# Optimization experiments

Measured on AMD Instinct MI355X. Metric: run time of the kernel, lower is better.

The kernel has to match this reference:

```python
import jax, jax.numpy as jnp
import numpy as np

B, N, D = 16, 8192, 768
H = int(D * 4.0)  # mlp hidden
EPS = 1e-6
D_SQRT = D ** (-0.5)


def setup_inputs() -> dict:
    key = jax.random.key(0)
    ks = jax.random.split(key, 6)
    x = jax.random.normal(ks[0], (B, N, D), dtype=jnp.float32)
    # learnable query, trunc-normal std = D**-0.5 (plain normal is fine for a reference)
    query = jax.random.normal(ks[1], (D,), dtype=jnp.float32) * D_SQRT
    ln_gamma = jnp.ones((D,), dtype=jnp.float32)
    ln_beta = jnp.zeros((D,), dtype=jnp.float32)
    w1 = jax.random.normal(ks[2], (D, H), dtype=jnp.float32) * (D ** -0.5)
    b1 = jnp.zeros((H,), dtype=jnp.float32)
    w2 = jax.random.normal(ks[3], (H, D), dtype=jnp.float32) * (H ** -0.5)
    b2 = jnp.zeros((D,), dtype=jnp.float32)
    return {"x": x, "query": query, "ln_gamma": ln_gamma, "ln_beta": ln_beta,
            "w1": w1, "b1": b1, "w2": w2, "b2": b2}


def _layernorm(x, gamma, beta):
    mu = jnp.mean(x, axis=-1, keepdims=True)
    var = jnp.mean(jnp.square(x - mu), axis=-1, keepdims=True)
    return (x - mu) * jax.lax.rsqrt(var + EPS) * gamma + beta


def reference(x, query, ln_gamma, ln_beta, w1, b1, w2, b2):
    # single-query cross attention: attn [B, N]
    attn = jnp.einsum('d,bnd->bn', query, x)
    attn_sm = jax.nn.softmax(attn * D_SQRT, axis=-1)
    pooled = jnp.einsum('bn,bnd->bd', attn_sm, x)  # [B, D]
    h = _layernorm(pooled, ln_gamma, ln_beta)
    h = jax.nn.gelu(h @ w1 + b1, approximate=False) @ w2 + b2
    out = pooled + h
    return out, attn
```

## Files before the change

### kernel.cpp

```cpp
#include <hip/hip_runtime.h>
#include <hip/hip_bf16.h>
#include <math.h>

#define BB 16
#define NN 8192
#define DD 768
#define HH 3072
#define EPSV 1e-6f
#define DSQRT 0.03608439182435161f

#define CHUNKS 64
#define ROWS_PER_BLOCK (NN / CHUNKS)
#define NWAVES 4
#define ROWS_PER_WAVE (ROWS_PER_BLOCK / NWAVES)
#define PSTRIDE 772
#define QQ 4

#define KS1 16
#define KL1 (DD / KS1)
#define KS2 48
#define KL2 (HH / KS2)

__global__ __launch_bounds__(256) void attn_pool_k(
    const float* __restrict__ x, const float* __restrict__ query,
    float* __restrict__ attn_out, float* __restrict__ partials)
{
    const int b     = blockIdx.y;
    const int chunk = blockIdx.x;
    const int tid   = threadIdx.x;
    const int wave  = tid >> 6;
    const int lane  = tid & 63;

    const float4* q4 = (const float4*)query;
    const float4 q0 = q4[lane];
    const float4 q1 = q4[lane + 64];
    const float4 q2 = q4[lane + 128];

    float4 p0 = make_float4(0.f, 0.f, 0.f, 0.f);
    float4 p1 = make_float4(0.f, 0.f, 0.f, 0.f);
    float4 p2 = make_float4(0.f, 0.f, 0.f, 0.f);
    float esum = 0.f;

    const int n0 = chunk * ROWS_PER_BLOCK + wave * ROWS_PER_WAVE;
    const float4* xb = (const float4*)(x + (size_t)b * NN * DD);

    #pragma unroll 2
    for (int r = 0; r < ROWS_PER_WAVE; ++r) {
        const int n = n0 + r;
        const float4* xr = xb + (size_t)n * (DD / 4);
        const float4 v0 = xr[lane];
        const float4 v1 = xr[lane + 64];
        const float4 v2 = xr[lane + 128];

        float s = v0.x * q0.x + v0.y * q0.y + v0.z * q0.z + v0.w * q0.w;
        s += v1.x * q1.x + v1.y * q1.y + v1.z * q1.z + v1.w * q1.w;
        s += v2.x * q2.x + v2.y * q2.y + v2.z * q2.z + v2.w * q2.w;
        #pragma unroll
        for (int off = 32; off > 0; off >>= 1) s += __shfl_xor(s, off);

        if (lane == 0) attn_out[(size_t)b * NN + n] = s;

        const float e = expf(s * DSQRT);
        esum += e;
        p0.x += e * v0.x; p0.y += e * v0.y; p0.z += e * v0.z; p0.w += e * v0.w;
        p1.x += e * v1.x; p1.y += e * v1.y; p1.z += e * v1.z; p1.w += e * v1.w;
        p2.x += e * v2.x; p2.y += e * v2.y; p2.z += e * v2.z; p2.w += e * v2.w;
    }

    __shared__ float lds[NWAVES][PSTRIDE];
    float* my = lds[wave];
    *(float4*)&my[lane * 4]       = p0;
    *(float4*)&my[256 + lane * 4] = p1;
    *(float4*)&my[512 + lane * 4] = p2;
    if (lane == 0) my[768] = esum;
    __syncthreads();

    float* outp = partials + (size_t)(b * CHUNKS + chunk) * PSTRIDE;
    #pragma unroll
    for (int k = 0; k < 3; ++k) {
        const int idx = tid + k * 256;
        outp[idx] = lds[0][idx] + lds[1][idx] + lds[2][idx] + lds[3][idx];
    }
    if (tid == 0) outp[768] = lds[0][768] + lds[1][768] + lds[2][768] + lds[3][768];
}

__global__ __launch_bounds__(256) void qreduce_k(
    const float* __restrict__ partials, float* __restrict__ qsum,
    float* __restrict__ qden)
{
    const int slice = blockIdx.x % 3;
    const int q     = blockIdx.x / 3;
    const int b     = blockIdx.y;
    const int tid   = threadIdx.x;
    const float* pb = partials + (size_t)b * CHUNKS * PSTRIDE;

    const int col = slice * 256 + tid;
    float s = 0.f;
    #pragma unroll
    for (int c = 0; c < CHUNKS / QQ; ++c)
        s += pb[(q * (CHUNKS / QQ) + c) * PSTRIDE + col];
    qsum[(size_t)(b * QQ + q) * DD + col] = s;

    if (slice == 0 && tid < CHUNKS / QQ) {
        float dn = pb[(q * (CHUNKS / QQ) + tid) * PSTRIDE + 768];
        #pragma unroll
        for (int off = 8; off > 0; off >>= 1) dn += __shfl_xor(dn, off, 16);
        if (tid == 0) qden[b * QQ + q] = dn;
    }
}

__global__ __launch_bounds__(768) void reduce_ln_k(
    const float* __restrict__ qsum, const float* __restrict__ qden,
    const float* __restrict__ gamma, const float* __restrict__ beta,
    float* __restrict__ pooled_ws, float* __restrict__ hln_ws)
{
    const int b = blockIdx.x, tid = threadIdx.x;

    float v = 0.f;
    #pragma unroll
    for (int q = 0; q < QQ; ++q) v += qsum[(size_t)(b * QQ + q) * DD + tid];

    const float den = qden[b * QQ] + qden[b * QQ + 1]
                    + qden[b * QQ + 2] + qden[b * QQ + 3];
    v *= (1.f / den);

    __shared__ float red[768];
    red[tid] = v;
    __syncthreads();
    if (tid < 256) red[tid] += red[tid + 256] + red[tid + 512];
    __syncthreads();
    for (int s = 128; s > 0; s >>= 1) {
        if (tid < s) red[tid] += red[tid + s];
        __syncthreads();
    }
    const float mu = red[0] * (1.f / 768.f);
    __syncthreads();

    const float dmu = v - mu;
    red[tid] = dmu * dmu;
    __syncthreads();
    if (tid < 256) red[tid] += red[tid + 256] + red[tid + 512];
    __syncthreads();
    for (int s = 128; s > 0; s >>= 1) {
        if (tid < s) red[tid] += red[tid + s];
        __syncthreads();
    }
    const float var = red[0] * (1.f / 768.f);
    const float rstd = rsqrtf(var + EPSV);

    pooled_ws[(size_t)b * DD + tid] = v;
    hln_ws[(size_t)b * DD + tid] = (v - mu) * rstd * gamma[tid] + beta[tid];
}

__global__ __launch_bounds__(256) void gemm1_part_k(
    const float* __restrict__ hln_ws, const float* __restrict__ w1,
    float* __restrict__ g1p)
{
    const int j  = blockIdx.x * 256 + threadIdx.x;
    const int k0 = blockIdx.y * KL1;

    __shared__ float hl[BB][KL1];
    for (int i = threadIdx.x; i < BB * KL1; i += 256) {
        const int b = i / KL1, d = i - b * KL1;
        hl[b][d] = hln_ws[(size_t)b * DD + k0 + d];
    }
    __syncthreads();

    float wv[KL1];
    #pragma unroll
    for (int d = 0; d < KL1; ++d) wv[d] = w1[(size_t)(k0 + d) * HH + j];

    float acc[BB];
    #pragma unroll
    for (int b = 0; b < BB; ++b) acc[b] = 0.f;

    #pragma unroll
    for (int d4 = 0; d4 < KL1 / 4; ++d4) {
        #pragma unroll
        for (int b = 0; b < BB; ++b) {
            const float4 h4 = *(const float4*)&hl[b][d4 * 4];
            acc[b] += h4.x * wv[d4 * 4] + h4.y * wv[d4 * 4 + 1]
                    + h4.z * wv[d4 * 4 + 2] + h4.w * wv[d4 * 4 + 3];
        }
    }

    float* op = g1p + (size_t)blockIdx.y * BB * HH;
    #pragma unroll
    for (int b = 0; b < BB; ++b) op[(size_t)b * HH + j] = acc[b];
}

__global__ __launch_bounds__(256) void comb1_gelu_k(
    const float* __restrict__ g1p, const float* __restrict__ b1,
    float* __restrict__ h1_ws)
{
    const int i = blockIdx.x * 256 + threadIdx.x;
    const int j = i % HH;

    float a = b1[j];
    #pragma unroll
    for (int s = 0; s < KS1; ++s) a += g1p[(size_t)s * BB * HH + i];
    h1_ws[i] = 0.5f * a * (1.f + erff(a * 0.70710678118654752f));
}

__global__ __launch_bounds__(256) void gemm2_part_k(
    const float* __restrict__ h1_ws, const float* __restrict__ w2,
    float* __restrict__ g2p)
{
    const int col = blockIdx.x * 256 + threadIdx.x;
    const int k0  = blockIdx.y * KL2;

    __shared__ float hg[BB][KL2];
    for (int i = threadIdx.x; i < BB * KL2; i += 256) {
        const int b = i / KL2, d = i - b * KL2;
        hg[b][d] = h1_ws[(size_t)b * HH + k0 + d];
    }
    __syncthreads();

    float wv[KL2];
    #pragma unroll
    for (int d = 0; d < KL2; ++d) wv[d] = w2[(size_t)(k0 + d) * DD + col];

    float acc[BB];
    #pragma unroll
    for (int b = 0; b < BB; ++b) acc[b] = 0.f;

    #pragma unroll
    for (int d4 = 0; d4 < KL2 / 4; ++d4) {
        #pragma unroll
        for (int b = 0; b < BB; ++b) {
            const float4 h4 = *(const float4*)&hg[b][d4 * 4];
            acc[b] += h4.x * wv[d4 * 4] + h4.y * wv[d4 * 4 + 1]
                    + h4.z * wv[d4 * 4 + 2] + h4.w * wv[d4 * 4 + 3];
        }
    }

    float* op = g2p + (size_t)blockIdx.y * BB * DD;
    #pragma unroll
    for (int b = 0; b < BB; ++b) op[(size_t)b * DD + col] = acc[b];
}

__global__ __launch_bounds__(256) void comb2_fin_k(
    const float* __restrict__ g2p, const float* __restrict__ pooled_ws,
    const float* __restrict__ b2, float* __restrict__ out)
{
    const int i = blockIdx.x * 256 + threadIdx.x;
    const int d = i % DD;

    float a = pooled_ws[i] + b2[d];
    #pragma unroll
    for (int s = 0; s < KS2; ++s) a += g2p[(size_t)s * BB * DD + i];
    out[i] = a;
}

extern "C" void kernel_launch(void* const* d_in, const int* in_sizes, int n_in,
                              void* d_out, int out_size, void* d_ws, size_t ws_size,
                              hipStream_t stream)
{
    const float* x     = (const float*)d_in[0];
    const float* query = (const float*)d_in[1];
    const float* gamma = (const float*)d_in[2];
    const float* beta  = (const float*)d_in[3];
    const float* w1    = (const float*)d_in[4];
    const float* b1    = (const float*)d_in[5];
    const float* w2    = (const float*)d_in[6];
    const float* b2    = (const float*)d_in[7];

    float* out      = (float*)d_out;
    float* attn_out = out + BB * DD;

    float* ws       = (float*)d_ws;
    float* partials = ws;
    float* qsum     = partials + BB * CHUNKS * PSTRIDE;
    float* qden     = qsum + BB * QQ * DD;
    float* pooled   = qden + 64;
    float* hln      = pooled + BB * DD;
    float* h1       = hln + BB * DD;
    float* g1p      = h1 + BB * HH;
    float* g2p      = g1p + KS1 * BB * HH;

    attn_pool_k<<<dim3(CHUNKS, BB), 256, 0, stream>>>(x, query, attn_out, partials);
    qreduce_k<<<dim3(12, BB), 256, 0, stream>>>(partials, qsum, qden);
    reduce_ln_k<<<dim3(BB), 768, 0, stream>>>(qsum, qden, gamma, beta, pooled, hln);
    gemm1_part_k<<<dim3(HH / 256, KS1), 256, 0, stream>>>(hln, w1, g1p);
    comb1_gelu_k<<<dim3(BB * HH / 256), 256, 0, stream>>>(g1p, b1, h1);
    gemm2_part_k<<<dim3(DD / 256, KS2), 256, 0, stream>>>(h1, w2, g2p);
    comb2_fin_k<<<dim3(BB * DD / 256), 256, 0, stream>>>(g2p, pooled, b2, out);
}
```

Before: 109.6 us.

## Fuse layernorm into qreduce via last-block atomic and fold GELU combine into GEMM2

The separate reduce_ln kernel is removed. The last qreduce block, detected with an atomic counter and thread fences, now computes pooled and the layernorm, using one wave per batch row. The split-K combine and GELU kernel is folded into the GEMM2 prologue, so each GEMM2 block rebuilds its slice of h1 from the g1p partials. This cuts two launches and one workspace round-trip, but adds a memset, a serial tail in a single block, and repeated g1p reads across the three column blocks.

```diff
diff --git a/kernel.cpp b/kernel.cpp
--- a/kernel.cpp
+++ b/kernel.cpp
@@ -84,72 +84,74 @@
     if (tid == 0) outp[768] = lds[0][768] + lds[1][768] + lds[2][768] + lds[3][768];
 }
 
-__global__ __launch_bounds__(256) void qreduce_k(
+__global__ __launch_bounds__(256) void qreduce_ln_k(
     const float* __restrict__ partials, float* __restrict__ qsum,
-    float* __restrict__ qden)
+    float* __restrict__ qden, const float* __restrict__ gamma,
+    const float* __restrict__ beta, float* __restrict__ pooled,
+    float* __restrict__ hln, int* __restrict__ qcnt)
 {
     const int slice = blockIdx.x % 3;
     const int q     = blockIdx.x / 3;
-    const int b     = blockIdx.y;
+    const int b0    = blockIdx.y;
     const int tid   = threadIdx.x;
-    const float* pb = partials + (size_t)b * CHUNKS * PSTRIDE;
-
-    const int col = slice * 256 + tid;
+    const float* pb = partials + (size_t)b0 * CHUNKS * PSTRIDE;
+
+    const int col0 = slice * 256 + tid;
     float s = 0.f;
     #pragma unroll
     for (int c = 0; c < CHUNKS / QQ; ++c)
-        s += pb[(q * (CHUNKS / QQ) + c) * PSTRIDE + col];
-    qsum[(size_t)(b * QQ + q) * DD + col] = s;
+        s += pb[(q * (CHUNKS / QQ) + c) * PSTRIDE + col0];
+    qsum[(size_t)(b0 * QQ + q) * DD + col0] = s;
 
     if (slice == 0 && tid < CHUNKS / QQ) {
         float dn = pb[(q * (CHUNKS / QQ) + tid) * PSTRIDE + 768];
         #pragma unroll
         for (int off = 8; off > 0; off >>= 1) dn += __shfl_xor(dn, off, 16);
-        if (tid == 0) qden[b * QQ + q] = dn;
-    }
-}
-
-__global__ __launch_bounds__(768) void reduce_ln_k(
-    const float* __restrict__ qsum, const float* __restrict__ qden,
-    const float* __restrict__ gamma, const float* __restrict__ beta,
-    float* __restrict__ pooled_ws, float* __restrict__ hln_ws)
-{
-    const int b = blockIdx.x, tid = threadIdx.x;
-
-    float v = 0.f;
-    #pragma unroll
-    for (int q = 0; q < QQ; ++q) v += qsum[(size_t)(b * QQ + q) * DD + tid];
-
-    const float den = qden[b * QQ] + qden[b * QQ + 1]
-                    + qden[b * QQ + 2] + qden[b * QQ + 3];
-    v *= (1.f / den);
-
-    __shared__ float red[768];
-    red[tid] = v;
-    __syncthreads();
-    if (tid < 256) red[tid] += red[tid + 256] + red[tid + 512];
-    __syncthreads();
-    for (int s = 128; s > 0; s >>= 1) {
-        if (tid < s) red[tid] += red[tid + s];
-        __syncthreads();
-    }
-    const float mu = red[0] * (1.f / 768.f);
-    __syncthreads();
-
-    const float dmu = v - mu;
-    red[tid] = dmu * dmu;
-    __syncthreads();
-    if (tid < 256) red[tid] += red[tid + 256] + red[tid + 512];
-    __syncthreads();
-    for (int s = 128; s > 0; s >>= 1) {
-        if (tid < s) red[tid] += red[tid + s];
-        __syncthreads();
-    }
-    const float var = red[0] * (1.f / 768.f);
-    const float rstd = rsqrtf(var + EPSV);
-
-    pooled_ws[(size_t)b * DD + tid] = v;
-    hln_ws[(size_t)b * DD + tid] = (v - mu) * rstd * gamma[tid] + beta[tid];
+        if (tid == 0) qden[b0 * QQ + q] = dn;
+    }
+
+    __threadfence();
+    __shared__ int s_last;
+    if (tid == 0) s_last = (atomicAdd(qcnt, 1) == 12 * BB - 1) ? 1 : 0;
+    __syncthreads();
+    if (!s_last) return;
+    __threadfence();
+
+    const int wave = tid >> 6, lane = tid & 63;
+    for (int b = wave; b < BB; b += 4) {
+        const float den = qden[b * QQ] + qden[b * QQ + 1]
+                        + qden[b * QQ + 2] + qden[b * QQ + 3];
+        const float inv = 1.f / den;
+        float v[12];
+        float sum = 0.f;
+        #pragma unroll
+        for (int c = 0; c < 12; ++c) {
+            const int col = c * 64 + lane;
+            float t = qsum[(size_t)(b * QQ + 0) * DD + col]
+                    + qsum[(size_t)(b * QQ + 1) * DD + col]
+                    + qsum[(size_t)(b * QQ + 2) * DD + col]
+                    + qsum[(size_t)(b * QQ + 3) * DD + col];
+            v[c] = t * inv;
+            sum += v[c];
+        }
+        #pragma unroll
+        for (int off = 32; off > 0; off >>= 1) sum += __shfl_xor(sum, off);
+        const float mu = sum * (1.f / 768.f);
+        float sq = 0.f;
+        #pragma unroll
+        for (int c = 0; c < 12; ++c) { const float d = v[c] - mu; sq += d * d; }
+        #pragma unroll
+        for (int off = 32; off > 0; off >>= 1) sq += __shfl_xor(sq, off);
+        const float rstd = rsqrtf(sq * (1.f / 768.f) + EPSV);
+        #pragma unroll
+        for (int c = 0; c < 12; ++c) {
+            const int col = c * 64 + lane;
+            pooled[(size_t)b * DD + col] = v[c];
+            hln[(size_t)b * DD + col] = (v[c] - mu) * rstd * gamma[col] + beta[col];
+        }
+    }
+    __syncthreads();
+    if (tid == 0) *qcnt = 0;
 }
 
 __global__ __launch_bounds__(256) void gemm1_part_k(
@@ -189,33 +191,26 @@
     for (int b = 0; b < BB; ++b) op[(size_t)b * HH + j] = acc[b];
 }
 
-__global__ __launch_bounds__(256) void comb1_gelu_k(
+__global__ __launch_bounds__(256) void gemm2_gelu_k(
     const float* __restrict__ g1p, const float* __restrict__ b1,
-    float* __restrict__ h1_ws)
-{
-    const int i = blockIdx.x * 256 + threadIdx.x;
-    const int j = i % HH;
-
-    float a = b1[j];
-    #pragma unroll
-    for (int s = 0; s < KS1; ++s) a += g1p[(size_t)s * BB * HH + i];
-    h1_ws[i] = 0.5f * a * (1.f + erff(a * 0.70710678118654752f));
-}
-
-__global__ __launch_bounds__(256) void gemm2_part_k(
-    const float* __restrict__ h1_ws, const float* __restrict__ w2,
-    float* __restrict__ g2p)
-{
-    const int col = blockIdx.x * 256 + threadIdx.x;
-    const int k0  = blockIdx.y * KL2;
+    const float* __restrict__ w2, float* __restrict__ g2p)
+{
+    const int cb  = blockIdx.x;
+    const int ks  = blockIdx.y;
+    const int k0  = ks * KL2;
+    const int tid = threadIdx.x;
 
     __shared__ float hg[BB][KL2];
-    for (int i = threadIdx.x; i < BB * KL2; i += 256) {
-        const int b = i / KL2, d = i - b * KL2;
-        hg[b][d] = h1_ws[(size_t)b * HH + k0 + d];
-    }
-    __syncthreads();
-
+    for (int i = tid; i < BB * KL2; i += 256) {
+        const int b = i / KL2, d = i - b * KL2, j = k0 + d;
+        float a = b1[j];
+        #pragma unroll
+        for (int s = 0; s < KS1; ++s) a += g1p[((size_t)s * BB + b) * HH + j];
+        hg[b][d] = 0.5f * a * (1.f + erff(a * 0.70710678118654752f));
+    }
+    __syncthreads();
+
+    const int col = cb * 256 + tid;
     float wv[KL2];
     #pragma unroll
     for (int d = 0; d < KL2; ++d) wv[d] = w2[(size_t)(k0 + d) * DD + col];
@@ -234,7 +229,7 @@
         }
     }
 
-    float* op = g2p + (size_t)blockIdx.y * BB * DD;
+    float* op = g2p + (size_t)ks * BB * DD;
     #pragma unroll
     for (int b = 0; b < BB; ++b) op[(size_t)b * DD + col] = acc[b];
 }
@@ -274,15 +269,15 @@
     float* qden     = qsum + BB * QQ * DD;
     float* pooled   = qden + 64;
     float* hln      = pooled + BB * DD;
-    float* h1       = hln + BB * DD;
-    float* g1p      = h1 + BB * HH;
+    float* g1p      = hln + BB * DD;
     float* g2p      = g1p + KS1 * BB * HH;
-
+    int*   qcnt     = (int*)(g2p + KS2 * BB * DD);
+
+    hipMemsetAsync(qcnt, 0, sizeof(int), stream);
     attn_pool_k<<<dim3(CHUNKS, BB), 256, 0, stream>>>(x, query, attn_out, partials);
-    qreduce_k<<<dim3(12, BB), 256, 0, stream>>>(partials, qsum, qden);
-    reduce_ln_k<<<dim3(BB), 768, 0, stream>>>(qsum, qden, gamma, beta, pooled, hln);
+    qreduce_ln_k<<<dim3(12, BB), 256, 0, stream>>>(partials, qsum, qden, gamma,
+                                                   beta, pooled, hln, qcnt);
     gemm1_part_k<<<dim3(HH / 256, KS1), 256, 0, stream>>>(hln, w1, g1p);
-    comb1_gelu_k<<<dim3(BB * HH / 256), 256, 0, stream>>>(g1p, b1, h1);
-    gemm2_part_k<<<dim3(DD / 256, KS2), 256, 0, stream>>>(h1, w2, g2p);
+    gemm2_gelu_k<<<dim3(DD / 256, KS2), 256, 0, stream>>>(g1p, b1, w2, g2p);
     comb2_fin_k<<<dim3(BB * DD / 256), 256, 0, stream>>>(g2p, pooled, b2, out);
 }
```

Result: slower. 130.8 us (+19.4%).
